# Optimization experiments

Measured on AMD Instinct MI355X. Metric: run time of the kernel, lower is better.

Reference implementation:

```python
import jax, jax.numpy as jnp
import numpy as np

WIDTH_POW = 9
WIDTH = 2 ** WIDTH_POW          # 512
HALF = WIDTH // 2               # 256
DEPTH = 32
BATCH = 65536
EPS = 0.01


def setup_inputs() -> dict:
    key = jax.random.key(0)
    k1, k2, k3, k4, k5, k6 = jax.random.split(key, 6)
    X = jax.random.normal(k1, (BATCH, WIDTH), dtype=jnp.float32)
    # butterfly rotation angles, one stage of depth-1 butterfly per layer
    thetas = jax.random.uniform(k2, (DEPTH, HALF), dtype=jnp.float32) * (2.0 * np.pi)
    # SmoothBendActivation params, init uniform in [-eps, eps]
    def u(k):
        return jax.random.uniform(k, (DEPTH, WIDTH), dtype=jnp.float32) * (2 * EPS) - EPS
    biases = u(k3)
    slopes1 = u(k4)
    slopes2 = u(k5)
    curvatures = u(k6)
    return {"X": X, "thetas": thetas, "biases": biases,
            "slopes1": slopes1, "slopes2": slopes2, "curvatures": curvatures}


def reference(X, thetas, biases, slopes1, slopes2, curvatures):
    B = X.shape[0]

    def step(x, p):
        theta, bias, s1, s2, curv = p
        # --- orthogonal butterfly rotation (depth 1) ---
        c = jnp.cos(theta)  # [HALF]
        s = jnp.sin(theta)
        x0 = x[:, :HALF]
        x1 = x[:, HALF:]
        n0 = x0 * c + x1 * s
        n1 = -x0 * s + x1 * c
        # fixed permutation perm[2j] = j, perm[2j+1] = j + HALF: interleave n0, n1
        x = jnp.stack([n0, n1], axis=-1).reshape(B, WIDTH)
        # --- smooth bend activation ---
        m1 = jnp.exp(s1)
        m2 = jnp.exp(s2)
        a = (m1 + m2) * 0.5
        cc = (m2 - m1) / (2.0 * a)
        b = jnp.sinh(bias)
        k = jnp.exp(curv)
        u = x * a - b
        x = u + cc * jnp.sqrt(u * u + 1.0 / k)
        return x, None

    out, _ = jax.lax.scan(step, X, (thetas, biases, slopes1, slopes2, curvatures))
    return out  # num_outputs == WIDTH, so no final slice needed
```

## Files before the change

kernel.cpp:

```cpp
#include <hip/hip_runtime.h>
#include <math.h>

#define WIDTH 512
#define HALF  256
#define DEPTH 32
#define BATCH 65536
#define RPW   8

__device__ float4 g_T1[DEPTH * WIDTH];
__device__ float  g_T2[DEPTH * WIDTH];

__global__ __launch_bounds__(256) void precompute_kernel(
    const float* __restrict__ thetas, const float* __restrict__ biases,
    const float* __restrict__ slopes1, const float* __restrict__ slopes2,
    const float* __restrict__ curvatures) {
  int tid = blockIdx.x * 256 + threadIdx.x;
  if (tid >= DEPTH * WIDTH) return;
  int d = tid >> 9;
  int p = tid & 511;
  int rot = (d + 1) % 9;
  int j = ((p << rot) | (p >> (9 - rot))) & 511;
  int i = j >> 1;
  int role = j & 1;
  float th = thetas[d * HALF + i];
  float c = cosf(th), s = sinf(th);
  float m1 = expf(slopes1[d * WIDTH + j]);
  float m2 = expf(slopes2[d * WIDTH + j]);
  float a  = 0.5f * (m1 + m2);
  float cc = (m2 - m1) / (m1 + m2);
  float b  = sinhf(biases[d * WIDTH + j]);
  float invk = expf(-curvatures[d * WIDTH + j]);
  float A = a * c;
  float S = role ? (-a * s) : (a * s);
  int q = d * WIDTH + ((p & 7) * 64 + (p >> 3));
  g_T1[q] = make_float4(A, S, b, cc);
  g_T2[q] = invk;
}

#if __has_builtin(__builtin_amdgcn_sqrtf)
#define FAST_SQRT(x) __builtin_amdgcn_sqrtf(x)
#else
#define FAST_SQRT(x) sqrtf(x)
#endif

__device__ __forceinline__ float stepf(float xs, float v, float4 P, float ik) {
  float u = fmaf(xs, P.x, fmaf(v, P.y, -P.z));
  float t = fmaf(u, u, ik);
  return fmaf(P.w, FAST_SQRT(t), u);
}

__device__ __forceinline__ void loadp(int d, int lane, float4 (&P)[8], float (&IK)[8]) {
  const float4* __restrict__ t1p = &g_T1[d * WIDTH + lane];
  const float*  __restrict__ t2p = &g_T2[d * WIDTH + lane];
#pragma unroll
  for (int s = 0; s < 8; ++s) { P[s] = t1p[s * 64]; IK[s] = t2p[s * 64]; }
}

template <int K>
__device__ __forceinline__ void do_layer(float (&x)[8][RPW], const float4 (&P)[8],
                                         const float (&IK)[8]) {
  if constexpr (K >= 3) {
    constexpr int m = 1 << (K - 3);
#pragma unroll
    for (int s = 0; s < 8; ++s) {
#pragma unroll
      for (int r = 0; r < RPW; ++r) {
        float xs = x[s][r];
        float v = __shfl_xor(xs, m, 64);
        x[s][r] = stepf(xs, v, P[s], IK[s]);
      }
    }
  } else {
    constexpr int SX = 1 << K;
#pragma unroll
    for (int s0 = 0; s0 < 8; ++s0) {
      if (s0 & SX) continue;
      constexpr int dummy = 0; (void)dummy;
      const int s1 = s0 | SX;
#pragma unroll
      for (int r = 0; r < RPW; ++r) {
        float v0 = x[s0][r], v1 = x[s1][r];
        float n0 = stepf(v0, v1, P[s0], IK[s0]);
        float n1 = stepf(v1, v0, P[s1], IK[s1]);
        x[s0][r] = n0;
        x[s1][r] = n1;
      }
    }
  }
}

__global__ __launch_bounds__(256) void net_kernel(const float* __restrict__ X,
                                                  float* __restrict__ out) {
  const int lane = threadIdx.x & 63;
  const int wv = blockIdx.x * 4 + (threadIdx.x >> 6);
  const size_t row0 = (size_t)wv * RPW;

  float x[8][RPW];
  const float4* __restrict__ Xv =
      reinterpret_cast<const float4*>(X + row0 * WIDTH);
#pragma unroll
  for (int r = 0; r < RPW; ++r) {
    float4 a = Xv[r * (WIDTH / 4) + lane * 2];
    float4 b = Xv[r * (WIDTH / 4) + lane * 2 + 1];
    x[0][r] = a.x; x[1][r] = a.y; x[2][r] = a.z; x[3][r] = a.w;
    x[4][r] = b.x; x[5][r] = b.y; x[6][r] = b.z; x[7][r] = b.w;
  }

  float4 P[8];
  float IK[8];
#define RUN_LAYER(DD)                                \
  do {                                               \
    if (d0 + DD < DEPTH) {                           \
      loadp(d0 + DD, lane, P, IK);                   \
      do_layer<8 - DD>(x, P, IK);                    \
    }                                                \
  } while (0)

  for (int d0 = 0; d0 < DEPTH; d0 += 9) {
    RUN_LAYER(0); RUN_LAYER(1); RUN_LAYER(2);
    RUN_LAYER(3); RUN_LAYER(4); RUN_LAYER(5);
    RUN_LAYER(6); RUN_LAYER(7); RUN_LAYER(8);
  }
#undef RUN_LAYER

  float* __restrict__ O = out + row0 * WIDTH;
#pragma unroll
  for (int s = 0; s < 8; ++s) {
    const int p = lane * 8 + s;
    const int cfin = ((p << 5) | (p >> 4)) & 511;
#pragma unroll
    for (int r = 0; r < RPW; ++r) O[r * WIDTH + cfin] = x[s][r];
  }
}

extern "C" void kernel_launch(void* const* d_in, const int* in_sizes, int n_in,
                              void* d_out, int out_size, void* d_ws, size_t ws_size,
                              hipStream_t stream) {
  const float* X          = (const float*)d_in[0];
  const float* thetas     = (const float*)d_in[1];
  const float* biases     = (const float*)d_in[2];
  const float* slopes1    = (const float*)d_in[3];
  const float* slopes2    = (const float*)d_in[4];
  const float* curvatures = (const float*)d_in[5];
  float* out = (float*)d_out;

  hipLaunchKernelGGL(precompute_kernel, dim3((DEPTH * WIDTH + 255) / 256),
                     dim3(256), 0, stream, thetas, biases, slopes1, slopes2,
                     curvatures);
  hipLaunchKernelGGL(net_kernel, dim3(BATCH / (RPW * 4)), dim3(256), 0, stream,
                     X, out);
}
```

Baseline: 217.9 us.

## Use packed float2 math across row pairs and halve rows per wave

Rows are processed in pairs as 2-wide float vectors so the FMAs can map to packed FP32 instructions (v_pk_fma_f32) on CDNA. The parameter tables are re-laid out with each value duplicated into paired lanes, and parameters are loaded per slot inside each layer. Rows per wave drop from 8 to 4, which doubles the grid and cuts register pressure so more waves can be resident. The trade-off is more parameter-load traffic per row, and sqrt and the shuffles still run as scalar ops.

```diff
diff --git a/kernel.cpp b/kernel.cpp
--- a/kernel.cpp
+++ b/kernel.cpp
@@ -5,10 +5,13 @@
 #define HALF  256
 #define DEPTH 32
 #define BATCH 65536
-#define RPW   8
+#define RPW   4
 
-__device__ float4 g_T1[DEPTH * WIDTH];
-__device__ float  g_T2[DEPTH * WIDTH];
+typedef float v2f __attribute__((ext_vector_type(2)));
+
+__device__ float4 g_AS[DEPTH * 8 * 64];
+__device__ float4 g_BC[DEPTH * 8 * 64];
+__device__ v2f    g_IK[DEPTH * 8 * 64];
 
 __global__ __launch_bounds__(256) void precompute_kernel(
     const float* __restrict__ thetas, const float* __restrict__ biases,
@@ -29,12 +32,14 @@
   float a  = 0.5f * (m1 + m2);
   float cc = (m2 - m1) / (m1 + m2);
   float b  = sinhf(biases[d * WIDTH + j]);
-  float invk = expf(-curvatures[d * WIDTH + j]);
+  float ik = expf(-curvatures[d * WIDTH + j]);
   float A = a * c;
   float S = role ? (-a * s) : (a * s);
-  int q = d * WIDTH + ((p & 7) * 64 + (p >> 3));
-  g_T1[q] = make_float4(A, S, b, cc);
-  g_T2[q] = invk;
+  int q = (d * 8 + (p & 7)) * 64 + (p >> 3);
+  g_AS[q] = make_float4(A, A, S, S);
+  g_BC[q] = make_float4(-b, -b, cc, cc);
+  v2f v; v.x = ik; v.y = ik;
+  g_IK[q] = v;
 }
 
 #if __has_builtin(__builtin_amdgcn_sqrtf)
@@ -43,47 +48,76 @@
 #define FAST_SQRT(x) sqrtf(x)
 #endif
 
-__device__ __forceinline__ float stepf(float xs, float v, float4 P, float ik) {
-  float u = fmaf(xs, P.x, fmaf(v, P.y, -P.z));
-  float t = fmaf(u, u, ik);
-  return fmaf(P.w, FAST_SQRT(t), u);
+__device__ __forceinline__ v2f vfma(v2f a, v2f b, v2f c) {
+#if __has_builtin(__builtin_elementwise_fma)
+  return __builtin_elementwise_fma(a, b, c);
+#else
+  v2f d;
+  d.x = fmaf(a.x, b.x, c.x);
+  d.y = fmaf(a.y, b.y, c.y);
+  return d;
+#endif
 }
 
-__device__ __forceinline__ void loadp(int d, int lane, float4 (&P)[8], float (&IK)[8]) {
-  const float4* __restrict__ t1p = &g_T1[d * WIDTH + lane];
-  const float*  __restrict__ t2p = &g_T2[d * WIDTH + lane];
-#pragma unroll
-  for (int s = 0; s < 8; ++s) { P[s] = t1p[s * 64]; IK[s] = t2p[s * 64]; }
+__device__ __forceinline__ v2f stepv(v2f xs, v2f v, v2f A, v2f S, v2f Bn,
+                                     v2f C, v2f IK) {
+  v2f u = vfma(xs, A, vfma(v, S, Bn));
+  v2f t = vfma(u, u, IK);
+  v2f q;
+  q.x = FAST_SQRT(t.x);
+  q.y = FAST_SQRT(t.y);
+  return vfma(C, q, u);
+}
+
+__device__ __forceinline__ v2f shflx(v2f x, int m) {
+  v2f r;
+  r.x = __shfl_xor(x.x, m, 64);
+  r.y = __shfl_xor(x.y, m, 64);
+  return r;
 }
 
 template <int K>
-__device__ __forceinline__ void do_layer(float (&x)[8][RPW], const float4 (&P)[8],
-                                         const float (&IK)[8]) {
+__device__ __forceinline__ void do_layer(int d, int lane, v2f (&x)[8][RPW / 2]) {
+  const int base = d * 512 + lane;
   if constexpr (K >= 3) {
-    constexpr int m = 1 << (K - 3);
+    const int m = 1 << (K - 3);
 #pragma unroll
     for (int s = 0; s < 8; ++s) {
+      float4 as = g_AS[base + s * 64];
+      float4 bc = g_BC[base + s * 64];
+      v2f ik = g_IK[base + s * 64];
+      v2f A, S, Bn, C;
+      A.x = as.x; A.y = as.y; S.x = as.z; S.y = as.w;
+      Bn.x = bc.x; Bn.y = bc.y; C.x = bc.z; C.y = bc.w;
 #pragma unroll
-      for (int r = 0; r < RPW; ++r) {
-        float xs = x[s][r];
-        float v = __shfl_xor(xs, m, 64);
-        x[s][r] = stepf(xs, v, P[s], IK[s]);
+      for (int h = 0; h < RPW / 2; ++h) {
+        v2f xs = x[s][h];
+        v2f v = shflx(xs, m);
+        x[s][h] = stepv(xs, v, A, S, Bn, C, ik);
       }
     }
   } else {
-    constexpr int SX = 1 << K;
+    const int SX = 1 << K;
 #pragma unroll
     for (int s0 = 0; s0 < 8; ++s0) {
       if (s0 & SX) continue;
-      constexpr int dummy = 0; (void)dummy;
       const int s1 = s0 | SX;
+      float4 as0 = g_AS[base + s0 * 64];
+      float4 bc0 = g_BC[base + s0 * 64];
+      v2f ik0 = g_IK[base + s0 * 64];
+      float4 as1 = g_AS[base + s1 * 64];
+      float4 bc1 = g_BC[base + s1 * 64];
+      v2f ik1 = g_IK[base + s1 * 64];
+      v2f A0, S0, Bn0, C0, A1, S1, Bn1, C1;
+      A0.x = as0.x; A0.y = as0.y; S0.x = as0.z; S0.y = as0.w;
+      Bn0.x = bc0.x; Bn0.y = bc0.y; C0.x = bc0.z; C0.y = bc0.w;
+      A1.x = as1.x; A1.y = as1.y; S1.x = as1.z; S1.y = as1.w;
+      Bn1.x = bc1.x; Bn1.y = bc1.y; C1.x = bc1.z; C1.y = bc1.w;
 #pragma unroll
-      for (int r = 0; r < RPW; ++r) {
-        float v0 = x[s0][r], v1 = x[s1][r];
-        float n0 = stepf(v0, v1, P[s0], IK[s0]);
-        float n1 = stepf(v1, v0, P[s1], IK[s1]);
-        x[s0][r] = n0;
-        x[s1][r] = n1;
+      for (int h = 0; h < RPW / 2; ++h) {
+        v2f v0 = x[s0][h], v1 = x[s1][h];
+        x[s0][h] = stepv(v0, v1, A0, S0, Bn0, C0, ik0);
+        x[s1][h] = stepv(v1, v0, A1, S1, Bn1, C1, ik1);
       }
     }
   }
@@ -95,25 +129,26 @@
   const int wv = blockIdx.x * 4 + (threadIdx.x >> 6);
   const size_t row0 = (size_t)wv * RPW;
 
-  float x[8][RPW];
+  v2f x[8][RPW / 2];
   const float4* __restrict__ Xv =
       reinterpret_cast<const float4*>(X + row0 * WIDTH);
 #pragma unroll
   for (int r = 0; r < RPW; ++r) {
     float4 a = Xv[r * (WIDTH / 4) + lane * 2];
     float4 b = Xv[r * (WIDTH / 4) + lane * 2 + 1];
-    x[0][r] = a.x; x[1][r] = a.y; x[2][r] = a.z; x[3][r] = a.w;
-    x[4][r] = b.x; x[5][r] = b.y; x[6][r] = b.z; x[7][r] = b.w;
+    float t[8] = {a.x, a.y, a.z, a.w, b.x, b.y, b.z, b.w};
+#pragma unroll
+    for (int s = 0; s < 8; ++s) {
+      if (r & 1) x[s][r >> 1].y = t[s];
+      else       x[s][r >> 1].x = t[s];
+    }
   }
 
-  float4 P[8];
-  float IK[8];
-#define RUN_LAYER(DD)                                \
-  do {                                               \
-    if (d0 + DD < DEPTH) {                           \
-      loadp(d0 + DD, lane, P, IK);                   \
-      do_layer<8 - DD>(x, P, IK);                    \
-    }                                                \
+#define RUN_LAYER(DD)                       \
+  do {                                      \
+    if (d0 + DD < DEPTH) {                  \
+      do_layer<8 - DD>(d0 + DD, lane, x);   \
+    }                                       \
   } while (0)
 
   for (int d0 = 0; d0 < DEPTH; d0 += 9) {
@@ -129,7 +164,10 @@
     const int p = lane * 8 + s;
     const int cfin = ((p << 5) | (p >> 4)) & 511;
 #pragma unroll
-    for (int r = 0; r < RPW; ++r) O[r * WIDTH + cfin] = x[s][r];
+    for (int h = 0; h < RPW / 2; ++h) {
+      O[(2 * h) * WIDTH + cfin]     = x[s][h].x;
+      O[(2 * h + 1) * WIDTH + cfin] = x[s][h].y;
+    }
   }
 }
 
```

After: 394.8 us. +81.2%, slower.
